# Performance work log

Hardware: AMD Instinct MI355X
Metric: run time of the kernel (lower is better)

The kernel has to match this reference:

```python
import jax, jax.numpy as jnp
import numpy as np

B, C, CO, H, W = 64, 64, 64, 56, 56
E, K = 8, 2


def _conv3x3(x, k, b):
    # x: [B,C,H,W], k: [CO,C,3,3], b: [CO]
    y = jax.lax.conv_general_dilated(
        x, k, window_strides=(1, 1), padding='SAME',
        dimension_numbers=('NCHW', 'OIHW', 'NCHW'))
    return y + b[None, :, None, None]


def setup_inputs() -> dict:
    key = jax.random.key(0)
    k1, k2, k3, k4, k5 = jax.random.split(key, 5)
    x = jax.random.normal(k1, (B, C, H, W), dtype=jnp.float32)
    weights = jax.random.uniform(k2, (B, K), dtype=jnp.float32)
    indices = jax.random.randint(k3, (B, K), 0, E, dtype=jnp.int32)
    W_exp = jax.random.normal(k4, (E, CO, C, 3, 3), dtype=jnp.float32) * 0.05
    b_exp = jax.random.normal(k5, (E, CO), dtype=jnp.float32) * 0.01
    return {'x': x, 'weights': weights, 'indices': indices,
            'W_exp': W_exp, 'b_exp': b_exp}


def reference(x, weights, indices, W_exp, b_exp):
    # Dense-equivalent MoE dispatch: run every expert on the full batch,
    # then gather the top-k expert outputs per sample and combine.
    # Same math as the masked gather / index_add_ loop in the torch module.
    # acts: [E, B, CO, H, W]
    acts = jax.vmap(lambda k, b: jax.nn.relu(_conv3x3(x, k, b)))(W_exp, b_exp)
    acts_b = jnp.transpose(acts, (1, 0, 2, 3, 4))  # [B, E, CO, H, W]
    idx = indices[:, :, None, None, None].astype(jnp.int32)
    sel = jnp.take_along_axis(acts_b, idx, axis=1)  # [B, K, CO, H, W]
    out = jnp.sum(sel * weights[:, :, None, None, None], axis=1)  # [B, CO, H, W]
    return out
```

## Files before the change

kernel.cpp:

```cpp
#include <hip/hip_runtime.h>


#define BB 64
#define CC 64
#define COO 64
#define HH 56
#define WW 56

typedef __bf16 bf16x8 __attribute__((ext_vector_type(8)));
typedef float  f32x4  __attribute__((ext_vector_type(4)));

__global__ __launch_bounds__(256) void prep_kernel(
    const float* __restrict__ x, const float* __restrict__ Wexp,
    __bf16* __restrict__ xT, __bf16* __restrict__ Wpack)
{
    const int bx  = blockIdx.x;
    const int tid = threadIdx.x;

    if (bx < 960) {
        __shared__ float tile[CC][WW + 1];
        const int b   = bx / 15;
        const int grp = bx - b * 15;
        #pragma unroll 1
        for (int rr = 0; rr < 4; ++rr) {
            const int hp = grp * 4 + rr;
            if (hp >= 58) break;
            __bf16* dst = xT + ((size_t)b * 58 + hp) * 4224;
            const bool interior = (hp >= 1 && hp <= HH);
            if (!interior) {
                bf16x8 z = {};
                for (int j = tid; j < 4224 / 8; j += 256)
                    *(bf16x8*)(dst + j * 8) = z;
                continue;
            }
            const int h = hp - 1;
            const float* xb = x + (size_t)b * CC * HH * WW + (size_t)h * WW;
            for (int i = tid; i < CC * 14; i += 256) {
                const int c = i / 14, wq = i - c * 14;
                const float4 f = *(const float4*)(xb + (size_t)c * HH * WW + wq * 4);
                tile[c][wq * 4 + 0] = f.x; tile[c][wq * 4 + 1] = f.y;
                tile[c][wq * 4 + 2] = f.z; tile[c][wq * 4 + 3] = f.w;
            }
            __syncthreads();
            for (int j = tid; j < 66 * 8; j += 256) {
                const int cg = j / 66;
                const int wc = j - cg * 66;
                bf16x8 v = {};
                if (wc >= 1 && wc <= WW) {
                    const int w = wc - 1;
                    #pragma unroll
                    for (int u = 0; u < 8; ++u)
                        v[u] = (__bf16)tile[cg * 8 + u][w];
                }
                *(bf16x8*)(dst + j * 8) = v;
            }
            __syncthreads();
        }
    } else {
        const int wp = bx - 960;
        const int e  = wp / 9, rs = wp - e * 9;
        const int r  = rs / 3, s  = rs - r * 3;
        for (int idx = tid; idx < 4096; idx += 256) {
            const int ks   = idx >> 11;
            const int rem  = idx & 2047;
            const int mt   = rem >> 9;
            const int lane = (rem >> 3) & 63;
            const int j    = idx & 7;
            const int co = mt * 16 + (lane & 15);
            const int c  = ks * 32 + ((lane >> 4) << 3) + j;
            const float v = Wexp[((((size_t)e * COO + co) * CC + c) * 3 + r) * 3 + s];
            Wpack[(size_t)e * 36864 + (size_t)rs * 4096 + idx] = (__bf16)v;
        }
    }
}

__global__ __launch_bounds__(256, 2) void moe_conv_mfma(
    const __bf16* __restrict__ xT, const __bf16* __restrict__ Wpack,
    const float* __restrict__ gate_w, const int* __restrict__ gate_i,
    const float* __restrict__ bexp, float* __restrict__ out)
{
    __shared__ __align__(16) __bf16 ldsA[72 * 512];

    const int bid = blockIdx.x;
    const int swz = (bid & 7) * 224 + (bid >> 3);
    const int b   = swz / 28;
    const int rem = swz - b * 28;
    const int h0  = (rem >> 1) * 4;
    const int mh  = rem & 1;

    const int tid = threadIdx.x;
    const int wid = tid >> 6, lane = tid & 63;
    const int n15 = lane & 15, quad = lane >> 4;
    const int wcol = wid * 16 + n15;

    const int   e0 = gate_i[b * 2 + 0], e1 = gate_i[b * 2 + 1];
    const float g0 = gate_w[b * 2 + 0], g1 = gate_w[b * 2 + 1];
    const __bf16* w0 = Wpack + (size_t)e0 * 36864;
    const __bf16* w1 = Wpack + (size_t)e1 * 36864;

    #pragma unroll
    for (int i = 0; i < 18; ++i) {
        const int q    = wid * 18 + i;
        const int rs   = q >> 3;
        const int rm   = q & 7;
        const int slot = rm >> 2, ks = (rm >> 1) & 1, mtl = rm & 1;
        const __bf16* src = (slot ? w1 : w0) + (size_t)rs * 4096
                          + ks * 2048 + (mh * 2 + mtl) * 512 + lane * 8;
        __bf16* dstp = &ldsA[q * 512 + lane * 8];
        __builtin_amdgcn_global_load_lds(
            (const __attribute__((address_space(1))) unsigned int*)src,
            (__attribute__((address_space(3))) unsigned int*)dstp, 16, 0, 0);
    }
    __syncthreads();

    const __bf16* pq = xT + (size_t)b * 244992 + quad * 528 + wcol * 8;

    f32x4 acc[2][2][4] = {};

    #pragma unroll
    for (int rs = 0; rs < 9; ++rs) {
        const int rn = rs / 3, sn = rs - rn * 3;
        const __bf16* pb = pq + (size_t)(h0 + rn) * 4224 + sn * 8;
        #pragma unroll
        for (int ks = 0; ks < 2; ++ks) {
            bf16x8 bf[4];
            #pragma unroll
            for (int t = 0; t < 4; ++t)
                bf[t] = *(const bf16x8*)(pb + t * 4224 + ks * 2112);
            #pragma unroll
            for (int slot = 0; slot < 2; ++slot) {
                #pragma unroll
                for (int mtl = 0; mtl < 2; ++mtl) {
                    const bf16x8 af = *(const bf16x8*)
                        &ldsA[(rs * 8 + slot * 4 + ks * 2 + mtl) * 512 + lane * 8];
                    #pragma unroll
                    for (int t = 0; t < 4; ++t)
                        acc[slot][mtl][t] = __builtin_amdgcn_mfma_f32_16x16x32_bf16(
                            af, bf[t], acc[slot][mtl][t], 0, 0, 0);
                }
            }
        }
    }

    if (wcol < WW) {
        #pragma unroll
        for (int t = 0; t < 4; ++t) {
            const int h = h0 + t;
            #pragma unroll
            for (int mtl = 0; mtl < 2; ++mtl) {
                #pragma unroll
                for (int v = 0; v < 4; ++v) {
                    const int co = (mh * 2 + mtl) * 16 + quad * 4 + v;
                    float a0 = acc[0][mtl][t][v] + bexp[e0 * COO + co];
                    float a1 = acc[1][mtl][t][v] + bexp[e1 * COO + co];
                    a0 = fmaxf(a0, 0.f);
                    a1 = fmaxf(a1, 0.f);
                    out[(((size_t)b * COO + co) * HH + h) * WW + wcol] =
                        g0 * a0 + g1 * a1;
                }
            }
        }
    }
}

extern "C" void kernel_launch(void* const* d_in, const int* in_sizes, int n_in,
                              void* d_out, int out_size, void* d_ws, size_t ws_size,
                              hipStream_t stream) {
    const float* x      = (const float*)d_in[0];
    const float* gate_w = (const float*)d_in[1];
    const int*   gate_i = (const int*)  d_in[2];
    const float* Wexp   = (const float*)d_in[3];
    const float* bexp   = (const float*)d_in[4];
    float* out = (float*)d_out;

    __bf16* Wpack = (__bf16*)d_ws;
    __bf16* xT    = (__bf16*)((char*)d_ws + 589824);

    prep_kernel<<<dim3(1032), 256, 0, stream>>>(x, Wexp, xT, Wpack);
    moe_conv_mfma<<<dim3(1792), 256, 0, stream>>>(xT, Wpack, gate_w, gate_i,
                                                  bexp, out);
}
```

Baseline: 147.9 us.

## Cover all output channels per block and double-buffer weight and input loads

Each block now computes all 64 output channels for its 4-row strip, so the launch uses half as many blocks and every input fragment feeds twice as many MFMAs. Weights are staged per (s, ks) step into two LDS buffers, and the input fragments are loaded with inline-asm global loads into register double buffers. This overlaps the next step's loads with the current step's MFMAs, and reuses the six loaded rows across the three filter rows. In exchange the accumulators double (128 floats) and register pressure rises, which may limit occupancy under launch_bounds(256,2), and the grid of 896 blocks is smaller.

```diff
diff --git a/kernel.cpp b/kernel.cpp
--- a/kernel.cpp
+++ b/kernel.cpp
@@ -79,14 +79,12 @@
     const float* __restrict__ gate_w, const int* __restrict__ gate_i,
     const float* __restrict__ bexp, float* __restrict__ out)
 {
-    __shared__ __align__(16) __bf16 ldsA[72 * 512];
+    __shared__ __align__(16) __bf16 ldsA[2 * 12288];
 
     const int bid = blockIdx.x;
-    const int swz = (bid & 7) * 224 + (bid >> 3);
-    const int b   = swz / 28;
-    const int rem = swz - b * 28;
-    const int h0  = (rem >> 1) * 4;
-    const int mh  = rem & 1;
+    const int swz = (bid & 7) * 112 + (bid >> 3);
+    const int b   = swz / 14;
+    const int h0  = (swz - b * 14) * 4;
 
     const int tid = threadIdx.x;
     const int wid = tid >> 6, lane = tid & 63;
@@ -98,48 +96,70 @@
     const __bf16* w0 = Wpack + (size_t)e0 * 36864;
     const __bf16* w1 = Wpack + (size_t)e1 * 36864;
 
+    auto stage = [&](int g, int bufn) {
+        const int s = g >> 1, ks = g & 1;
+        #pragma unroll
+        for (int i = 0; i < 6; ++i) {
+            const int ch = wid * 6 + i;
+            const int r = ch >> 3, rm = ch & 7;
+            const int slot = rm >> 2, mt = rm & 3;
+            const __bf16* src = (slot ? w1 : w0) + (size_t)(r * 3 + s) * 4096
+                              + ks * 2048 + mt * 512 + lane * 8;
+            __bf16* dstp = &ldsA[bufn * 12288 + ch * 512 + lane * 8];
+            __builtin_amdgcn_global_load_lds(
+                (const __attribute__((address_space(1))) unsigned int*)src,
+                (__attribute__((address_space(3))) unsigned int*)dstp, 16, 0, 0);
+        }
+    };
+
+    const __bf16* pqh = xT + (size_t)b * 244992 + (size_t)h0 * 4224
+                      + quad * 528 + wcol * 8;
+
+    f32x4 acc[2][4][4] = {};
+    f32x4 bfb[2][6];
+
+    auto issueB = [&](int g, int bufn) {
+        const int s = g >> 1, ks = g & 1;
+        #pragma unroll
+        for (int t = 0; t < 6; ++t) {
+            const __bf16* a = pqh + (size_t)t * 4224 + s * 8 + ks * 2112;
+            asm volatile("global_load_dwordx4 %0, %1, off"
+                         : "=&v"(bfb[bufn][t]) : "v"(a));
+        }
+    };
+
+    stage(0, 0);
+    issueB(0, 0);
+
     #pragma unroll
-    for (int i = 0; i < 18; ++i) {
-        const int q    = wid * 18 + i;
-        const int rs   = q >> 3;
-        const int rm   = q & 7;
-        const int slot = rm >> 2, ks = (rm >> 1) & 1, mtl = rm & 1;
-        const __bf16* src = (slot ? w1 : w0) + (size_t)rs * 4096
-                          + ks * 2048 + (mh * 2 + mtl) * 512 + lane * 8;
-        __bf16* dstp = &ldsA[q * 512 + lane * 8];
-        __builtin_amdgcn_global_load_lds(
-            (const __attribute__((address_space(1))) unsigned int*)src,
-            (__attribute__((address_space(3))) unsigned int*)dstp, 16, 0, 0);
-    }
-    __syncthreads();
-
-    const __bf16* pq = xT + (size_t)b * 244992 + quad * 528 + wcol * 8;
-
-    f32x4 acc[2][2][4] = {};
-
-    #pragma unroll
-    for (int rs = 0; rs < 9; ++rs) {
-        const int rn = rs / 3, sn = rs - rn * 3;
-        const __bf16* pb = pq + (size_t)(h0 + rn) * 4224 + sn * 8;
-        #pragma unroll
-        for (int ks = 0; ks < 2; ++ks) {
-            bf16x8 bf[4];
-            #pragma unroll
-            for (int t = 0; t < 4; ++t)
-                bf[t] = *(const bf16x8*)(pb + t * 4224 + ks * 2112);
+    for (int g = 0; g < 6; ++g) {
+        const int buf = g & 1;
+        asm volatile("s_waitcnt vmcnt(0)" ::: "memory");
+        __builtin_amdgcn_sched_barrier(0);
+        __builtin_amdgcn_s_barrier();
+        __builtin_amdgcn_sched_barrier(0);
+        if (g < 5) { stage(g + 1, buf ^ 1); issueB(g + 1, buf ^ 1); }
+        __builtin_amdgcn_sched_barrier(0);
+
+        __builtin_amdgcn_s_setprio(1);
+        #pragma unroll
+        for (int r = 0; r < 3; ++r) {
             #pragma unroll
             for (int slot = 0; slot < 2; ++slot) {
                 #pragma unroll
-                for (int mtl = 0; mtl < 2; ++mtl) {
+                for (int mt = 0; mt < 4; ++mt) {
                     const bf16x8 af = *(const bf16x8*)
-                        &ldsA[(rs * 8 + slot * 4 + ks * 2 + mtl) * 512 + lane * 8];
+                        &ldsA[buf * 12288 + (r * 8 + slot * 4 + mt) * 512
+                              + lane * 8];
                     #pragma unroll
                     for (int t = 0; t < 4; ++t)
-                        acc[slot][mtl][t] = __builtin_amdgcn_mfma_f32_16x16x32_bf16(
-                            af, bf[t], acc[slot][mtl][t], 0, 0, 0);
+                        acc[slot][mt][t] = __builtin_amdgcn_mfma_f32_16x16x32_bf16(
+                            af, __builtin_bit_cast(bf16x8, bfb[buf][r + t]),
+                            acc[slot][mt][t], 0, 0, 0);
                 }
             }
         }
+        __builtin_amdgcn_s_setprio(0);
     }
 
     if (wcol < WW) {
@@ -147,12 +167,12 @@
         for (int t = 0; t < 4; ++t) {
             const int h = h0 + t;
             #pragma unroll
-            for (int mtl = 0; mtl < 2; ++mtl) {
+            for (int mt = 0; mt < 4; ++mt) {
                 #pragma unroll
                 for (int v = 0; v < 4; ++v) {
-                    const int co = (mh * 2 + mtl) * 16 + quad * 4 + v;
-                    float a0 = acc[0][mtl][t][v] + bexp[e0 * COO + co];
-                    float a1 = acc[1][mtl][t][v] + bexp[e1 * COO + co];
+                    const int co = mt * 16 + quad * 4 + v;
+                    float a0 = acc[0][mt][t][v] + bexp[e0 * COO + co];
+                    float a1 = acc[1][mt][t][v] + bexp[e1 * COO + co];
                     a0 = fmaxf(a0, 0.f);
                     a1 = fmaxf(a1, 0.f);
                     out[(((size_t)b * COO + co) * HH + h) * WW + wcol] =
@@ -177,6 +197,6 @@
     __bf16* xT    = (__bf16*)((char*)d_ws + 589824);
 
     prep_kernel<<<dim3(1032), 256, 0, stream>>>(x, Wexp, xT, Wpack);
-    moe_conv_mfma<<<dim3(1792), 256, 0, stream>>>(xT, Wpack, gate_w, gate_i,
-                                                  bexp, out);
+    moe_conv_mfma<<<dim3(896), 256, 0, stream>>>(xT, Wpack, gate_w, gate_i,
+                                                 bexp, out);
 }
```

Result: no change. 150.5 us (+1.8%).
